# Performance work log

Measured on AMD Instinct MI355X. Metric: run time of the kernel, lower is better.

Reference implementation:

```python
import jax, jax.numpy as jnp
import numpy as np

B, L, H, D, N, R, K = 1, 2048, 2048, 4096, 16, 128, 4


def setup_inputs() -> dict:
    key = jax.random.key(0)
    ks = jax.random.split(key, 10)
    s = 0.02
    x = jax.random.normal(ks[0], (B, L, H), dtype=jnp.float32)
    W_in = jax.random.normal(ks[1], (H, 2 * D), dtype=jnp.float32) * s
    conv_w = jax.random.normal(ks[2], (K, D), dtype=jnp.float32) * s  # depthwise causal conv
    conv_b = jnp.zeros((D,), dtype=jnp.float32)
    W_x = jax.random.normal(ks[3], (D, R + 2 * N), dtype=jnp.float32) * s
    W_dt = jax.random.normal(ks[4], (R, D), dtype=jnp.float32) * (R ** -0.5)
    # dt bias initialized so softplus(b_dt) ~ dt in [1e-3, 1e-1]
    dt = jnp.exp(jax.random.uniform(ks[5], (D,)) * (np.log(0.1) - np.log(1e-3)) + np.log(1e-3))
    b_dt = dt + jnp.log(-jnp.expm1(-dt))
    A_log = jnp.broadcast_to(jnp.log(jnp.arange(1, N + 1, dtype=jnp.float32)), (D, N))
    D_param = jnp.ones((D,), dtype=jnp.float32)
    W_out = jax.random.normal(ks[6], (D, H), dtype=jnp.float32) * s
    return {"x": x, "W_in": W_in, "conv_w": conv_w, "conv_b": conv_b,
            "W_x": W_x, "W_dt": W_dt, "b_dt": b_dt, "A_log": A_log,
            "D_param": D_param, "W_out": W_out}


def _mamba_fwd(x, W_in, conv_w, conv_b, W_x, W_dt, b_dt, A_log, D_param, W_out):
    silu = jax.nn.silu
    # in_proj then chunk into hidden / gate: [B,L,D] each
    proj = x @ W_in
    hs, gate = jnp.split(proj, 2, axis=-1)
    # causal depthwise conv along sequence (pad K-1 on the left)
    hs_pad = jnp.pad(hs, ((0, 0), (K - 1, 0), (0, 0)))
    conv = sum(hs_pad[:, k:k + L, :] * conv_w[k] for k in range(K)) + conv_b
    hs = silu(conv)  # [B,L,D]
    # ssm parameters
    ssm_p = hs @ W_x  # [B,L,R+2N]
    dt_in, Bm, Cm = jnp.split(ssm_p, [R, R + N], axis=-1)
    dt = jax.nn.softplus(dt_in @ W_dt + b_dt)  # [B,L,D]
    A = -jnp.exp(A_log)  # [D,N]
    dA = jnp.exp(dt[..., None] * A)                       # [B,L,D,N]
    dBu = dt[..., None] * Bm[:, :, None, :] * hs[..., None]  # [B,L,D,N]

    def step(s, inp):
        dA_t, dBu_t, C_t = inp
        s = dA_t * s + dBu_t                 # [B,D,N]
        y = jnp.einsum('bdn,bn->bd', s, C_t)
        return s, y

    s0 = jnp.zeros((B, D, N), dtype=x.dtype)
    xs = (jnp.moveaxis(dA, 1, 0), jnp.moveaxis(dBu, 1, 0), jnp.moveaxis(Cm, 1, 0))
    _, ys = jax.lax.scan(step, s0, xs)       # [L,B,D]
    y = jnp.moveaxis(ys, 0, 1)               # [B,L,D]
    y = y + hs * D_param
    y = y * silu(gate)
    return y @ W_out                          # [B,L,H]


def reference(x, W_in, conv_w, conv_b, W_x, W_dt, b_dt, A_log, D_param, W_out):
    return _mamba_fwd(x, W_in, conv_w, conv_b, W_x, W_dt, b_dt, A_log, D_param, W_out)
```

## Files before the change

kernel.cpp:

```cpp
#include <hip/hip_runtime.h>
#include <hip/hip_bf16.h>

typedef short short8 __attribute__((ext_vector_type(8)));
typedef float floatx4 __attribute__((ext_vector_type(4)));
using bf16 = __hip_bfloat16;

static constexpr int L = 2048, H = 2048, D = 4096, NS = 16, R = 128, KC = 4;
static constexpr int CCH = 64, TCH = L / CCH;
static constexpr int KSP = 16, KCHUNK = 4096 / KSP;

__device__ __forceinline__ void g2lds16(const void* g, void* l) {
  __builtin_amdgcn_global_load_lds((const __attribute__((address_space(1))) unsigned int*)g,
                                   (__attribute__((address_space(3))) unsigned int*)l,
                                   16, 0, 0);
}

__global__ void cast_f2b(const float* __restrict__ in, bf16* __restrict__ out, int n) {
  int i = blockIdx.x * 256 + threadIdx.x;
  if (i < n) out[i] = __float2bfloat16(in[i]);
}

__global__ void transpose_cast(const float* __restrict__ in, bf16* __restrict__ out,
                               int Rr, int Cc) {
  __shared__ float tile[32][33];
  int c0 = blockIdx.x * 32, r0 = blockIdx.y * 32;
  int tx = threadIdx.x, ty = threadIdx.y;
#pragma unroll
  for (int i = 0; i < 32; i += 8)
    tile[ty + i][tx] = in[(size_t)(r0 + ty + i) * Cc + (c0 + tx)];
  __syncthreads();
#pragma unroll
  for (int i = 0; i < 32; i += 8)
    out[(size_t)(c0 + ty + i) * Rr + (r0 + tx)] = __float2bfloat16(tile[tx][ty + i]);
}

__global__ __launch_bounds__(256) void gemm_async(
    const bf16* __restrict__ A, int lda,
    const bf16* __restrict__ Bt, int ldb,
    float* __restrict__ C, int ldc, int K) {
  __shared__ short As[128 * 32];
  __shared__ short Bs[128 * 32];
  const int m0 = blockIdx.y * 128, n0 = blockIdx.x * 128;
  const int tid = threadIdx.x;
  const int lane = tid & 63;
  const int wave = tid >> 6;
  const int wm = (wave >> 1) * 64, wn = (wave & 1) * 64;
  const int lr = lane & 15, kq = lane >> 4;
  const int sr = lane >> 2, sc = (lane & 3) * 8;

  const bf16* Ab = A + (size_t)(m0 + wave * 16 + sr) * lda + sc;
  const bf16* Bb = Bt + (size_t)(n0 + wave * 16 + sr) * ldb + sc;
  short* Asw = &As[wave * 16 * 32];
  short* Bsw = &Bs[wave * 16 * 32];

  floatx4 acc[4][4];
#pragma unroll
  for (int i = 0; i < 4; i++)
#pragma unroll
    for (int j = 0; j < 4; j++)
#pragma unroll
      for (int r = 0; r < 4; r++) acc[i][j][r] = 0.f;

  for (int k0 = 0; k0 < K; k0 += 32) {
    __syncthreads();
#pragma unroll
    for (int j = 0; j < 2; j++) {
      g2lds16(Ab + (size_t)j * 64 * lda + k0, Asw + j * 64 * 32);
      g2lds16(Bb + (size_t)j * 64 * ldb + k0, Bsw + j * 64 * 32);
    }
    __syncthreads();
    short8 af[4], bfr[4];
#pragma unroll
    for (int i = 0; i < 4; i++)
      af[i] = *(const short8*)(&As[(wm + i * 16 + lr) * 32 + kq * 8]);
#pragma unroll
    for (int j = 0; j < 4; j++)
      bfr[j] = *(const short8*)(&Bs[(wn + j * 16 + lr) * 32 + kq * 8]);
#pragma unroll
    for (int i = 0; i < 4; i++)
#pragma unroll
      for (int j = 0; j < 4; j++)
        acc[i][j] = __builtin_amdgcn_mfma_f32_16x16x32_bf16(af[i], bfr[j], acc[i][j], 0, 0, 0);
  }

  const int rb = kq * 4;
#pragma unroll
  for (int i = 0; i < 4; i++)
#pragma unroll
    for (int j = 0; j < 4; j++) {
      int col = n0 + wn + j * 16 + lr;
      int row = m0 + wm + i * 16 + rb;
#pragma unroll
      for (int r = 0; r < 4; r++)
        C[(size_t)(row + r) * ldc + col] = acc[i][j][r];
    }
}

__global__ __launch_bounds__(256) void gemm_splitk(
    const bf16* __restrict__ A, int lda,
    const bf16* __restrict__ Bt, int ldb,
    float* __restrict__ P, int ldc, int N) {
  __shared__ short As[128 * 40];
  __shared__ short Bs[128 * 40];
  const int m0 = blockIdx.y * 128, n0 = blockIdx.x * 128;
  const int kbeg = blockIdx.z * KCHUNK;
  float* C = P + (size_t)blockIdx.z * 2048 * ldc;
  const int tid = threadIdx.x;
  const int lane = tid & 63;
  const int wave = tid >> 6;
  const int wm = (wave >> 1) * 64, wn = (wave & 1) * 64;
  const int lr = lane & 15, kq = lane >> 4;
  const int srow = tid >> 2, scol = (tid & 3) * 8;

  floatx4 acc[4][4];
#pragma unroll
  for (int i = 0; i < 4; i++)
#pragma unroll
    for (int j = 0; j < 4; j++)
#pragma unroll
      for (int r = 0; r < 4; r++) acc[i][j][r] = 0.f;

  for (int k0 = kbeg; k0 < kbeg + KCHUNK; k0 += 32) {
    __syncthreads();
#pragma unroll
    for (int h = 0; h < 2; h++) {
      int r = srow + h * 64;
      short8 va = *(const short8*)((const short*)A + (size_t)(m0 + r) * lda + k0 + scol);
      *(short8*)(&As[r * 40 + scol]) = va;
    }
#pragma unroll
    for (int h = 0; h < 2; h++) {
      int r = srow + h * 64;
      short8 vb;
      if ((n0 + r) < N) {
        vb = *(const short8*)((const short*)Bt + (size_t)(n0 + r) * ldb + k0 + scol);
      } else {
#pragma unroll
        for (int q = 0; q < 8; q++) vb[q] = 0;
      }
      *(short8*)(&Bs[r * 40 + scol]) = vb;
    }
    __syncthreads();
    short8 af[4], bfr[4];
#pragma unroll
    for (int i = 0; i < 4; i++)
      af[i] = *(const short8*)(&As[(wm + i * 16 + lr) * 40 + kq * 8]);
#pragma unroll
    for (int j = 0; j < 4; j++)
      bfr[j] = *(const short8*)(&Bs[(wn + j * 16 + lr) * 40 + kq * 8]);
#pragma unroll
    for (int i = 0; i < 4; i++)
#pragma unroll
      for (int j = 0; j < 4; j++)
        acc[i][j] = __builtin_amdgcn_mfma_f32_16x16x32_bf16(af[i], bfr[j], acc[i][j], 0, 0, 0);
  }

  const int rb = kq * 4;
#pragma unroll
  for (int i = 0; i < 4; i++)
#pragma unroll
    for (int j = 0; j < 4; j++) {
      int col = n0 + wn + j * 16 + lr;
      if (col >= N) continue;
      int row = m0 + wm + i * 16 + rb;
#pragma unroll
      for (int r = 0; r < 4; r++)
        C[(size_t)(row + r) * ldc + col] = acc[i][j][r];
    }
}

__global__ void splitk_reduce(const float* __restrict__ P, float* __restrict__ ssmp,
                              bf16* __restrict__ dtin) {
  int idx = blockIdx.x * 256 + threadIdx.x;
  float s = 0.f;
#pragma unroll
  for (int z = 0; z < KSP; z++) s += P[(size_t)z * 2048 * 160 + idx];
  ssmp[idx] = s;
  int t = idx / 160, c = idx - t * 160;
  if (c < R) dtin[t * R + c] = __float2bfloat16(s);
}

__global__ void conv_silu(const float* __restrict__ proj,
                          const float* __restrict__ conv_w, const float* __restrict__ conv_b,
                          bf16* __restrict__ hs_b) {
  int idx = blockIdx.x * 256 + threadIdx.x;
  int d = idx & (D - 1), t = idx >> 12;
  float acc = conv_b[d];
#pragma unroll
  for (int k = 0; k < KC; k++) {
    int tt = t + k - (KC - 1);
    if (tt >= 0) acc += proj[(size_t)tt * (2 * D) + d] * conv_w[k * D + d];
  }
  float s = acc / (1.f + __expf(-acc));
  hs_b[idx] = __float2bfloat16(s);
}

__device__ __forceinline__ float softplusf(float v) {
  return (v > 20.f) ? v : log1pf(__expf(v));
}

__global__ __launch_bounds__(256) void scan_phase1(
    const float* __restrict__ dtraw, const float* __restrict__ b_dt,
    const bf16* __restrict__ hs_b, const float* __restrict__ ssmp,
    const float* __restrict__ A_log,
    float* __restrict__ sdt_out, float* __restrict__ S_out) {
  const int d = blockIdx.x * 256 + threadIdx.x;
  const int c = blockIdx.y;
  float An[NS];
#pragma unroll
  for (int n = 0; n < NS; n++) An[n] = -__expf(A_log[d * NS + n]);
  const float bdt = b_dt[d];
  float s[NS];
#pragma unroll
  for (int n = 0; n < NS; n++) s[n] = 0.f;
  float sdt = 0.f;
  const int t0 = c * TCH;
#pragma unroll 2
  for (int t = t0; t < t0 + TCH; t++) {
    float dtv = softplusf(dtraw[(size_t)t * D + d] + bdt);
    float hsv = __bfloat162float(hs_b[(size_t)t * D + d]);
    sdt += dtv;
    float u = dtv * hsv;
    const float* Bp = ssmp + (size_t)t * 160 + 128;
#pragma unroll
    for (int n = 0; n < NS; n++) {
      float dA = __expf(An[n] * dtv);
      s[n] = dA * s[n] + Bp[n] * u;
    }
  }
  sdt_out[(size_t)c * D + d] = sdt;
  float* Sp = S_out + ((size_t)c * D + d) * NS;
#pragma unroll
  for (int n = 0; n < NS; n += 4)
    *(floatx4*)(Sp + n) = *(floatx4*)(s + n);
}

__global__ __launch_bounds__(256) void scan_phase2(
    const float* __restrict__ sdt, const float* __restrict__ S,
    const float* __restrict__ A_log, float* __restrict__ I) {
  int g = blockIdx.x * 256 + threadIdx.x;
  int d = g >> 4;
  float An = -__expf(A_log[g]);
  float cur = 0.f;
  for (int c = 0; c < CCH; c++) {
    I[(size_t)c * D * NS + g] = cur;
    cur = __expf(An * sdt[(size_t)c * D + d]) * cur + S[(size_t)c * D * NS + g];
  }
}

__global__ __launch_bounds__(256) void scan_phase3(
    const float* __restrict__ dtraw, const float* __restrict__ b_dt,
    const bf16* __restrict__ hs_b, const float* __restrict__ ssmp,
    const float* __restrict__ proj, const float* __restrict__ A_log,
    const float* __restrict__ D_param, const float* __restrict__ I,
    bf16* __restrict__ y_b) {
  const int d = blockIdx.x * 256 + threadIdx.x;
  const int c = blockIdx.y;
  float An[NS];
#pragma unroll
  for (int n = 0; n < NS; n++) An[n] = -__expf(A_log[d * NS + n]);
  const float bdt = b_dt[d];
  const float Dp = D_param[d];
  float s[NS];
  const float* Ip = I + ((size_t)c * D + d) * NS;
#pragma unroll
  for (int n = 0; n < NS; n += 4)
    *(floatx4*)(s + n) = *(const floatx4*)(Ip + n);
  const int t0 = c * TCH;
#pragma unroll 2
  for (int t = t0; t < t0 + TCH; t++) {
    float dtv = softplusf(dtraw[(size_t)t * D + d] + bdt);
    float hsv = __bfloat162float(hs_b[(size_t)t * D + d]);
    float u = dtv * hsv;
    const float* Bp = ssmp + (size_t)t * 160 + 128;
    const float* Cp = ssmp + (size_t)t * 160 + 144;
    float y = 0.f;
#pragma unroll
    for (int n = 0; n < NS; n++) {
      float dA = __expf(An[n] * dtv);
      s[n] = dA * s[n] + Bp[n] * u;
      y += s[n] * Cp[n];
    }
    float gv = proj[(size_t)t * (2 * D) + D + d];
    float yv = (y + hsv * Dp) * (gv / (1.f + __expf(-gv)));
    y_b[(size_t)t * D + d] = __float2bfloat16(yv);
  }
}

extern "C" void kernel_launch(void* const* d_in, const int* in_sizes, int n_in,
                              void* d_out, int out_size, void* d_ws, size_t ws_size,
                              hipStream_t stream) {
  const float* x      = (const float*)d_in[0];
  const float* W_in   = (const float*)d_in[1];
  const float* conv_w = (const float*)d_in[2];
  const float* conv_b = (const float*)d_in[3];
  const float* W_x    = (const float*)d_in[4];
  const float* W_dt   = (const float*)d_in[5];
  const float* b_dt   = (const float*)d_in[6];
  const float* A_log  = (const float*)d_in[7];
  const float* D_par  = (const float*)d_in[8];
  const float* W_out  = (const float*)d_in[9];
  float* outp = (float*)d_out;

  char* ws = (char*)d_ws;
  size_t off = 0;
  auto alloc = [&](size_t bytes) {
    char* p = ws + off;
    off += (bytes + 255) & ~(size_t)255;
    return (void*)p;
  };
  float* proj   = (float*)alloc((size_t)L * 2 * D * 4);
  bf16*  hs_b   = (bf16*) alloc((size_t)L * D * 2);
  float* ssmp   = (float*)alloc((size_t)L * 160 * 4);
  bf16*  dtin_b = (bf16*) alloc((size_t)L * R * 2);
  float* dtbuf  = (float*)alloc((size_t)L * D * 4);
  bf16*  y_b    = (bf16*) alloc((size_t)L * D * 2);
  bf16*  x_b    = (bf16*) alloc((size_t)L * H * 2);
  bf16*  WinT   = (bf16*) alloc((size_t)2 * D * H * 2);
  bf16*  WoutT  = (bf16*) alloc((size_t)H * D * 2);
  bf16*  WxT    = (bf16*) alloc((size_t)160 * D * 2);
  bf16*  WdtT   = (bf16*) alloc((size_t)D * R * 2);
  float* sdt    = (float*)alloc((size_t)CCH * D * 4);
  float* Sbuf   = (float*)alloc((size_t)CCH * D * NS * 4);
  float* Ibuf   = (float*)alloc((size_t)CCH * D * NS * 4);
  float* part   = (float*)alloc((size_t)KSP * L * 160 * 4);

  cast_f2b<<<(L * H) / 256, 256, 0, stream>>>(x, x_b, L * H);

  dim3 tb(32, 8);
  transpose_cast<<<dim3((2 * D) / 32, H / 32), tb, 0, stream>>>(W_in, WinT, H, 2 * D);
  transpose_cast<<<dim3(H / 32, D / 32), tb, 0, stream>>>(W_out, WoutT, D, H);
  transpose_cast<<<dim3(160 / 32, D / 32), tb, 0, stream>>>(W_x, WxT, D, 160);
  transpose_cast<<<dim3(D / 32, R / 32), tb, 0, stream>>>(W_dt, WdtT, R, D);

  gemm_async<<<dim3((2 * D) / 128, L / 128), 256, 0, stream>>>(
      x_b, H, WinT, H, proj, 2 * D, H);
  conv_silu<<<(L * D) / 256, 256, 0, stream>>>(proj, conv_w, conv_b, hs_b);
  gemm_splitk<<<dim3(2, L / 128, KSP), 256, 0, stream>>>(
      hs_b, D, WxT, D, part, 160, 160);
  splitk_reduce<<<(L * 160) / 256, 256, 0, stream>>>(part, ssmp, dtin_b);
  gemm_async<<<dim3(D / 128, L / 128), 256, 0, stream>>>(
      dtin_b, R, WdtT, R, dtbuf, D, R);

  scan_phase1<<<dim3(D / 256, CCH), 256, 0, stream>>>(
      dtbuf, b_dt, hs_b, ssmp, A_log, sdt, Sbuf);
  scan_phase2<<<(D * NS) / 256, 256, 0, stream>>>(sdt, Sbuf, A_log, Ibuf);
  scan_phase3<<<dim3(D / 256, CCH), 256, 0, stream>>>(
      dtbuf, b_dt, hs_b, ssmp, proj, A_log, D_par, Ibuf, y_b);

  gemm_async<<<dim3(H / 128, L / 128), 256, 0, stream>>>(
      y_b, D, WoutT, D, outp, H, D);
}
```

Baseline: 537.3 us.

## Store intermediates in bf16, split-K the output GEMM, prefetch in chunk scan

The in-projection GEMM now writes the hidden half as bf16 and the gate half as fp32 into separate buffers, and the dt projection GEMM writes bf16. This cuts the bytes written and read by the conv and scan kernels. The final out-projection GEMM is split four ways along K into partial buffers that reuse dead workspace, followed by a vectorised reduction, so more blocks run on the device. The phase-2 scan prefetches the next chunk's values. In exchange, dt and the pre-conv hidden state lose precision, and the split-K path adds extra partial-sum traffic.

```diff
diff --git a/kernel.cpp b/kernel.cpp
--- a/kernel.cpp
+++ b/kernel.cpp
@@ -8,6 +8,7 @@
 static constexpr int L = 2048, H = 2048, D = 4096, NS = 16, R = 128, KC = 4;
 static constexpr int CCH = 64, TCH = L / CCH;
 static constexpr int KSP = 16, KCHUNK = 4096 / KSP;
+static constexpr int ZOUT = 4, KOUT = 4096 / ZOUT;
 
 __device__ __forceinline__ void g2lds16(const void* g, void* l) {
   __builtin_amdgcn_global_load_lds((const __attribute__((address_space(1))) unsigned int*)g,
@@ -34,10 +35,11 @@
     out[(size_t)(c0 + ty + i) * Rr + (r0 + tx)] = __float2bfloat16(tile[tx][ty + i]);
 }
 
+template <int MODE>
 __global__ __launch_bounds__(256) void gemm_async(
     const bf16* __restrict__ A, int lda,
     const bf16* __restrict__ Bt, int ldb,
-    float* __restrict__ C, int ldc, int K) {
+    float* __restrict__ Cf, bf16* __restrict__ Cb, int ldc, int K) {
   __shared__ short As[128 * 32];
   __shared__ short Bs[128 * 32];
   const int m0 = blockIdx.y * 128, n0 = blockIdx.x * 128;
@@ -91,9 +93,92 @@
       int col = n0 + wn + j * 16 + lr;
       int row = m0 + wm + i * 16 + rb;
 #pragma unroll
+      for (int r = 0; r < 4; r++) {
+        float v = acc[i][j][r];
+        if (MODE == 0) {
+          Cf[(size_t)(row + r) * ldc + col] = v;
+        } else if (MODE == 1) {
+          Cb[(size_t)(row + r) * ldc + col] = __float2bfloat16(v);
+        } else {
+          if (col < D) Cb[(size_t)(row + r) * D + col] = __float2bfloat16(v);
+          else         Cf[(size_t)(row + r) * D + col - D] = v;
+        }
+      }
+    }
+}
+
+__global__ __launch_bounds__(256) void gemm_async_splitk(
+    const bf16* __restrict__ A, int lda,
+    const bf16* __restrict__ Bt, int ldb,
+    float* __restrict__ P, int ldc, int kch) {
+  __shared__ short As[128 * 32];
+  __shared__ short Bs[128 * 32];
+  const int m0 = blockIdx.y * 128, n0 = blockIdx.x * 128;
+  const int kbeg = blockIdx.z * kch;
+  float* C = P + (size_t)blockIdx.z * L * ldc;
+  const int tid = threadIdx.x;
+  const int lane = tid & 63;
+  const int wave = tid >> 6;
+  const int wm = (wave >> 1) * 64, wn = (wave & 1) * 64;
+  const int lr = lane & 15, kq = lane >> 4;
+  const int sr = lane >> 2, sc = (lane & 3) * 8;
+
+  const bf16* Ab = A + (size_t)(m0 + wave * 16 + sr) * lda + sc;
+  const bf16* Bb = Bt + (size_t)(n0 + wave * 16 + sr) * ldb + sc;
+  short* Asw = &As[wave * 16 * 32];
+  short* Bsw = &Bs[wave * 16 * 32];
+
+  floatx4 acc[4][4];
+#pragma unroll
+  for (int i = 0; i < 4; i++)
+#pragma unroll
+    for (int j = 0; j < 4; j++)
+#pragma unroll
+      for (int r = 0; r < 4; r++) acc[i][j][r] = 0.f;
+
+  for (int k0 = kbeg; k0 < kbeg + kch; k0 += 32) {
+    __syncthreads();
+#pragma unroll
+    for (int j = 0; j < 2; j++) {
+      g2lds16(Ab + (size_t)j * 64 * lda + k0, Asw + j * 64 * 32);
+      g2lds16(Bb + (size_t)j * 64 * ldb + k0, Bsw + j * 64 * 32);
+    }
+    __syncthreads();
+    short8 af[4], bfr[4];
+#pragma unroll
+    for (int i = 0; i < 4; i++)
+      af[i] = *(const short8*)(&As[(wm + i * 16 + lr) * 32 + kq * 8]);
+#pragma unroll
+    for (int j = 0; j < 4; j++)
+      bfr[j] = *(const short8*)(&Bs[(wn + j * 16 + lr) * 32 + kq * 8]);
+#pragma unroll
+    for (int i = 0; i < 4; i++)
+#pragma unroll
+      for (int j = 0; j < 4; j++)
+        acc[i][j] = __builtin_amdgcn_mfma_f32_16x16x32_bf16(af[i], bfr[j], acc[i][j], 0, 0, 0);
+  }
+
+  const int rb = kq * 4;
+#pragma unroll
+  for (int i = 0; i < 4; i++)
+#pragma unroll
+    for (int j = 0; j < 4; j++) {
+      int col = n0 + wn + j * 16 + lr;
+      int row = m0 + wm + i * 16 + rb;
+#pragma unroll
       for (int r = 0; r < 4; r++)
         C[(size_t)(row + r) * ldc + col] = acc[i][j][r];
     }
+}
+
+__global__ void out_reduce(const float* __restrict__ P, float* __restrict__ out) {
+  int i = blockIdx.x * 256 + threadIdx.x;
+  const int LH4 = L * H / 4;
+  const floatx4* P4 = (const floatx4*)P;
+  floatx4 s = P4[i];
+#pragma unroll
+  for (int z = 1; z < ZOUT; z++) s += P4[(size_t)z * LH4 + i];
+  ((floatx4*)out)[i] = s;
 }
 
 __global__ __launch_bounds__(256) void gemm_splitk(
@@ -104,7 +189,7 @@
   __shared__ short Bs[128 * 40];
   const int m0 = blockIdx.y * 128, n0 = blockIdx.x * 128;
   const int kbeg = blockIdx.z * KCHUNK;
-  float* C = P + (size_t)blockIdx.z * 2048 * ldc;
+  float* C = P + (size_t)blockIdx.z * L * ldc;
   const int tid = threadIdx.x;
   const int lane = tid & 63;
   const int wave = tid >> 6;
@@ -174,13 +259,13 @@
   int idx = blockIdx.x * 256 + threadIdx.x;
   float s = 0.f;
 #pragma unroll
-  for (int z = 0; z < KSP; z++) s += P[(size_t)z * 2048 * 160 + idx];
+  for (int z = 0; z < KSP; z++) s += P[(size_t)z * L * 160 + idx];
   ssmp[idx] = s;
   int t = idx / 160, c = idx - t * 160;
   if (c < R) dtin[t * R + c] = __float2bfloat16(s);
 }
 
-__global__ void conv_silu(const float* __restrict__ proj,
+__global__ void conv_silu(const bf16* __restrict__ projh,
                           const float* __restrict__ conv_w, const float* __restrict__ conv_b,
                           bf16* __restrict__ hs_b) {
   int idx = blockIdx.x * 256 + threadIdx.x;
@@ -189,7 +274,7 @@
 #pragma unroll
   for (int k = 0; k < KC; k++) {
     int tt = t + k - (KC - 1);
-    if (tt >= 0) acc += proj[(size_t)tt * (2 * D) + d] * conv_w[k * D + d];
+    if (tt >= 0) acc += __bfloat162float(projh[(size_t)tt * D + d]) * conv_w[k * D + d];
   }
   float s = acc / (1.f + __expf(-acc));
   hs_b[idx] = __float2bfloat16(s);
@@ -200,7 +285,7 @@
 }
 
 __global__ __launch_bounds__(256) void scan_phase1(
-    const float* __restrict__ dtraw, const float* __restrict__ b_dt,
+    const bf16* __restrict__ dtraw, const float* __restrict__ b_dt,
     const bf16* __restrict__ hs_b, const float* __restrict__ ssmp,
     const float* __restrict__ A_log,
     float* __restrict__ sdt_out, float* __restrict__ S_out) {
@@ -217,7 +302,7 @@
   const int t0 = c * TCH;
 #pragma unroll 2
   for (int t = t0; t < t0 + TCH; t++) {
-    float dtv = softplusf(dtraw[(size_t)t * D + d] + bdt);
+    float dtv = softplusf(__bfloat162float(dtraw[(size_t)t * D + d]) + bdt);
     float hsv = __bfloat162float(hs_b[(size_t)t * D + d]);
     sdt += dtv;
     float u = dtv * hsv;
@@ -242,16 +327,23 @@
   int d = g >> 4;
   float An = -__expf(A_log[g]);
   float cur = 0.f;
+  float sdt_n = sdt[d];
+  float S_n = S[g];
   for (int c = 0; c < CCH; c++) {
+    float sdt_c = sdt_n, S_c = S_n;
+    if (c + 1 < CCH) {
+      sdt_n = sdt[(size_t)(c + 1) * D + d];
+      S_n = S[(size_t)(c + 1) * D * NS + g];
+    }
     I[(size_t)c * D * NS + g] = cur;
-    cur = __expf(An * sdt[(size_t)c * D + d]) * cur + S[(size_t)c * D * NS + g];
+    cur = __expf(An * sdt_c) * cur + S_c;
   }
 }
 
 __global__ __launch_bounds__(256) void scan_phase3(
-    const float* __restrict__ dtraw, const float* __restrict__ b_dt,
+    const bf16* __restrict__ dtraw, const float* __restrict__ b_dt,
     const bf16* __restrict__ hs_b, const float* __restrict__ ssmp,
-    const float* __restrict__ proj, const float* __restrict__ A_log,
+    const float* __restrict__ gate_f, const float* __restrict__ A_log,
     const float* __restrict__ D_param, const float* __restrict__ I,
     bf16* __restrict__ y_b) {
   const int d = blockIdx.x * 256 + threadIdx.x;
@@ -269,7 +361,7 @@
   const int t0 = c * TCH;
 #pragma unroll 2
   for (int t = t0; t < t0 + TCH; t++) {
-    float dtv = softplusf(dtraw[(size_t)t * D + d] + bdt);
+    float dtv = softplusf(__bfloat162float(dtraw[(size_t)t * D + d]) + bdt);
     float hsv = __bfloat162float(hs_b[(size_t)t * D + d]);
     float u = dtv * hsv;
     const float* Bp = ssmp + (size_t)t * 160 + 128;
@@ -281,7 +373,7 @@
       s[n] = dA * s[n] + Bp[n] * u;
       y += s[n] * Cp[n];
     }
-    float gv = proj[(size_t)t * (2 * D) + D + d];
+    float gv = gate_f[(size_t)t * D + d];
     float yv = (y + hsv * Dp) * (gv / (1.f + __expf(-gv)));
     y_b[(size_t)t * D + d] = __float2bfloat16(yv);
   }
@@ -309,21 +401,24 @@
     off += (bytes + 255) & ~(size_t)255;
     return (void*)p;
   };
-  float* proj   = (float*)alloc((size_t)L * 2 * D * 4);
-  bf16*  hs_b   = (bf16*) alloc((size_t)L * D * 2);
-  float* ssmp   = (float*)alloc((size_t)L * 160 * 4);
-  bf16*  dtin_b = (bf16*) alloc((size_t)L * R * 2);
-  float* dtbuf  = (float*)alloc((size_t)L * D * 4);
-  bf16*  y_b    = (bf16*) alloc((size_t)L * D * 2);
-  bf16*  x_b    = (bf16*) alloc((size_t)L * H * 2);
-  bf16*  WinT   = (bf16*) alloc((size_t)2 * D * H * 2);
-  bf16*  WoutT  = (bf16*) alloc((size_t)H * D * 2);
-  bf16*  WxT    = (bf16*) alloc((size_t)160 * D * 2);
+  float* gate_f  = (float*)alloc((size_t)L * D * 4);
+  bf16*  hs_b    = (bf16*) alloc((size_t)L * D * 2);
+  float* ssmp    = (float*)alloc((size_t)L * 160 * 4);
+  bf16*  dtin_b  = (bf16*) alloc((size_t)L * R * 2);
+  bf16*  dtbuf_b = (bf16*) alloc((size_t)L * D * 2);
+  bf16*  y_b     = (bf16*) alloc((size_t)L * D * 2);
+  bf16*  WoutT   = (bf16*) alloc((size_t)H * D * 2);
+  float* sdt     = (float*)alloc((size_t)CCH * D * 4);
+  float* Sbuf    = (float*)alloc((size_t)CCH * D * NS * 4);
+  float* Ibuf    = (float*)alloc((size_t)CCH * D * NS * 4);
+  size_t tbase = off;
+  bf16*  x_b     = (bf16*) alloc((size_t)L * H * 2);
+  bf16*  WinT    = (bf16*) alloc((size_t)2 * D * H * 2);
+  bf16*  WxT     = (bf16*) alloc((size_t)160 * D * 2);
   bf16*  WdtT   = (bf16*) alloc((size_t)D * R * 2);
-  float* sdt    = (float*)alloc((size_t)CCH * D * 4);
-  float* Sbuf   = (float*)alloc((size_t)CCH * D * NS * 4);
-  float* Ibuf   = (float*)alloc((size_t)CCH * D * NS * 4);
-  float* part   = (float*)alloc((size_t)KSP * L * 160 * 4);
+  bf16*  projh_b = (bf16*) alloc((size_t)L * D * 2);
+  float* part    = (float*)alloc((size_t)KSP * L * 160 * 4);
+  float* part2   = (float*)(ws + tbase);
 
   cast_f2b<<<(L * H) / 256, 256, 0, stream>>>(x, x_b, L * H);
 
@@ -333,21 +428,22 @@
   transpose_cast<<<dim3(160 / 32, D / 32), tb, 0, stream>>>(W_x, WxT, D, 160);
   transpose_cast<<<dim3(D / 32, R / 32), tb, 0, stream>>>(W_dt, WdtT, R, D);
 
-  gemm_async<<<dim3((2 * D) / 128, L / 128), 256, 0, stream>>>(
-      x_b, H, WinT, H, proj, 2 * D, H);
-  conv_silu<<<(L * D) / 256, 256, 0, stream>>>(proj, conv_w, conv_b, hs_b);
+  gemm_async<2><<<dim3((2 * D) / 128, L / 128), 256, 0, stream>>>(
+      x_b, H, WinT, H, gate_f, projh_b, D, H);
+  conv_silu<<<(L * D) / 256, 256, 0, stream>>>(projh_b, conv_w, conv_b, hs_b);
   gemm_splitk<<<dim3(2, L / 128, KSP), 256, 0, stream>>>(
       hs_b, D, WxT, D, part, 160, 160);
   splitk_reduce<<<(L * 160) / 256, 256, 0, stream>>>(part, ssmp, dtin_b);
-  gemm_async<<<dim3(D / 128, L / 128), 256, 0, stream>>>(
-      dtin_b, R, WdtT, R, dtbuf, D, R);
+  gemm_async<1><<<dim3(D / 128, L / 128), 256, 0, stream>>>(
+      dtin_b, R, WdtT, R, nullptr, dtbuf_b, D, R);
 
   scan_phase1<<<dim3(D / 256, CCH), 256, 0, stream>>>(
-      dtbuf, b_dt, hs_b, ssmp, A_log, sdt, Sbuf);
+      dtbuf_b, b_dt, hs_b, ssmp, A_log, sdt, Sbuf);
   scan_phase2<<<(D * NS) / 256, 256, 0, stream>>>(sdt, Sbuf, A_log, Ibuf);
   scan_phase3<<<dim3(D / 256, CCH), 256, 0, stream>>>(
-      dtbuf, b_dt, hs_b, ssmp, proj, A_log, D_par, Ibuf, y_b);
-
-  gemm_async<<<dim3(H / 128, L / 128), 256, 0, stream>>>(
-      y_b, D, WoutT, D, outp, H, D);
-}
+      dtbuf_b, b_dt, hs_b, ssmp, gate_f, A_log, D_par, Ibuf, y_b);
+
+  gemm_async_splitk<<<dim3(H / 128, L / 128, ZOUT), 256, 0, stream>>>(
+      y_b, D, WoutT, D, part2, H, KOUT);
+  out_reduce<<<(L * H / 4) / 256, 256, 0, stream>>>(part2, outp);
+}
```

Result: no change. 538.5 us (+0.2%).
